# Kernel optimization log

Measured on AMD Instinct MI355X. Metric: run time of the kernel, lower is better.

## Reference

```python
import jax, jax.numpy as jnp
import numpy as np

OUT_FEATURES = 4096
IN_FEATURES = 4096
NUMEL = OUT_FEATURES * IN_FEATURES          # 16777216
NUM_SUPER = NUMEL // 256                    # 65536 superblocks of 256 weights


def setup_inputs() -> dict:
    key = jax.random.key(0)
    k_x, k_p, k_d, k_dm, k_s, k_m = jax.random.split(key, 6)
    x = jax.random.normal(k_x, (2, 2048, IN_FEATURES), dtype=jnp.float32)
    # packed bytes: two 4-bit quants per byte
    packed = jax.random.randint(k_p, (NUMEL // 2,), 0, 256, dtype=jnp.int32)
    # per-superblock fp scale/min (small positive values like real Q4_K 'd'/'dmin')
    d = jax.random.uniform(k_d, (NUM_SUPER,), dtype=jnp.float32) * 0.02
    dmin = jax.random.uniform(k_dm, (NUM_SUPER,), dtype=jnp.float32) * 0.02
    # per-subblock 6-bit scale/min quants (8 subblocks per superblock)
    scales = jax.random.randint(k_s, (NUM_SUPER * 8,), 0, 64, dtype=jnp.int32)
    mins = jax.random.randint(k_m, (NUM_SUPER * 8,), 0, 64, dtype=jnp.int32)
    return {"x": x, "packed": packed, "d": d, "dmin": dmin,
            "scales": scales, "mins": mins}


def _q4_k_dequantize(packed, d, dmin, scales, mins):
    # nibble split: low then high, interleaved per byte (stack dim=1 + flatten)
    low = packed & 15
    high = (packed >> 4) & 15
    q = jnp.stack([low, high], axis=1).reshape(-1).astype(jnp.float32)  # [NUMEL]
    blocks = q.reshape(NUM_SUPER, 8, 32)
    blk_scale = (scales.astype(jnp.float32) / 63.0).reshape(NUM_SUPER, 8, 1)
    blk_min = (mins.astype(jnp.float32) / 63.0).reshape(NUM_SUPER, 8, 1)
    normalized = blocks / 15.0 * blk_scale + blk_min
    w = normalized * d.reshape(NUM_SUPER, 1, 1) + dmin.reshape(NUM_SUPER, 1, 1)
    return w.reshape(OUT_FEATURES, IN_FEATURES)


def reference(x, packed, d, dmin, scales, mins):
    w = _q4_k_dequantize(packed, d, dmin, scales, mins).astype(x.dtype)
    # F.linear(x, w) = x @ w.T ; bias is None
    return jnp.einsum('bsk,nk->bsn', x, w)
```

## Files before the change

kernel.cpp:

```cpp
#include <hip/hip_runtime.h>
#include <stdint.h>

#define M_DIM 4096
#define K_DIM 4096
#define N_DIM 4096

typedef float f32x4 __attribute__((ext_vector_type(4)));
typedef int   i32x4 __attribute__((ext_vector_type(4)));

__global__ __launch_bounds__(256) void quant_x(const float* __restrict__ x,
                                               int8_t* __restrict__ xq,
                                               float* __restrict__ sx) {
    __shared__ float red[4];
    const int row  = blockIdx.x;
    const int base = threadIdx.x * 16;
    const float* xr = x + (size_t)row * K_DIM + base;
    float4 v[4];
#pragma unroll
    for (int c = 0; c < 4; ++c) v[c] = ((const float4*)xr)[c];
    float am = 0.f;
#pragma unroll
    for (int c = 0; c < 4; ++c) {
        am = fmaxf(am, fabsf(v[c].x)); am = fmaxf(am, fabsf(v[c].y));
        am = fmaxf(am, fabsf(v[c].z)); am = fmaxf(am, fabsf(v[c].w));
    }
#pragma unroll
    for (int off = 32; off; off >>= 1) am = fmaxf(am, __shfl_xor(am, off, 64));
    if ((threadIdx.x & 63) == 0) red[threadIdx.x >> 6] = am;
    __syncthreads();
    float amax = fmaxf(fmaxf(red[0], red[1]), fmaxf(red[2], red[3]));
    amax = fmaxf(amax, 1e-20f);
    const float inv = 127.0f / amax;
    int ow[4];
#pragma unroll
    for (int c = 0; c < 4; ++c) {
        int q0 = __float2int_rn(v[c].x * inv);
        int q1 = __float2int_rn(v[c].y * inv);
        int q2 = __float2int_rn(v[c].z * inv);
        int q3 = __float2int_rn(v[c].w * inv);
        ow[c] = (q0 & 255) | ((q1 & 255) << 8) | ((q2 & 255) << 16) | ((q3 & 255) << 24);
    }
    ((int4*)(xq + (size_t)row * K_DIM + base))[0] = make_int4(ow[0], ow[1], ow[2], ow[3]);
    if (threadIdx.x == 0) sx[row] = amax / 127.0f;
}

__global__ __launch_bounds__(256) void quant_w(const int* __restrict__ packed,
                                               const float* __restrict__ d,
                                               const float* __restrict__ dmin,
                                               const int* __restrict__ scales,
                                               const int* __restrict__ mins,
                                               int8_t* __restrict__ wq,
                                               float* __restrict__ sw) {
    __shared__ float sa[128], sb[128], red[4];
    const int n = blockIdx.x;
    const int t = threadIdx.x;
    float m = 0.f;
    if (t < 128) {
        int sub  = n * 128 + t;
        int sidx = n * 16 + (t >> 3);
        float dd = d[sidx], dm = dmin[sidx];
        float a = dd * (float)scales[sub] * (1.0f / 945.0f);
        float b = dd * (float)mins[sub] * (1.0f / 63.0f) + dm;
        sa[t] = a; sb[t] = b;
        m = 15.0f * a + b;
    }
#pragma unroll
    for (int off = 32; off; off >>= 1) m = fmaxf(m, __shfl_xor(m, off, 64));
    if ((t & 63) == 0) red[t >> 6] = m;
    __syncthreads();
    float rowmax = fmaxf(fmaxf(red[0], red[1]), fmaxf(red[2], red[3]));
    rowmax = fmaxf(rowmax, 1e-20f);
    const float inv = 127.0f / rowmax;

    const int sub = t >> 1;
    const float a = sa[sub] * inv;
    const float b = sb[sub] * inv;
    const int4* p4 = (const int4*)(packed + (size_t)n * (K_DIM / 2) + t * 8);
    int4 pv0 = p4[0], pv1 = p4[1];
    int bytes[8] = {pv0.x, pv0.y, pv0.z, pv0.w, pv1.x, pv1.y, pv1.z, pv1.w};
    int ow[4];
#pragma unroll
    for (int c = 0; c < 4; ++c) {
        int b0 = bytes[2 * c], b1 = bytes[2 * c + 1];
        int q0 = __float2int_rn((float)(b0 & 15) * a + b);
        int q1 = __float2int_rn((float)((b0 >> 4) & 15) * a + b);
        int q2 = __float2int_rn((float)(b1 & 15) * a + b);
        int q3 = __float2int_rn((float)((b1 >> 4) & 15) * a + b);
        ow[c] = (q0 & 255) | ((q1 & 255) << 8) | ((q2 & 255) << 16) | ((q3 & 255) << 24);
    }
    ((int4*)(wq + (size_t)n * K_DIM + t * 16))[0] = make_int4(ow[0], ow[1], ow[2], ow[3]);
    if (t == 0) sw[n] = rowmax / 127.0f;
}

#define BK 128

__device__ __forceinline__ void async_copy16(void* lds, const void* g) {
    __builtin_amdgcn_global_load_lds(
        (const __attribute__((address_space(1))) void*)g,
        (__attribute__((address_space(3))) void*)lds, 16, 0, 0);
}

#define BARRIER() asm volatile("s_barrier" ::: "memory")
#define LGKM0()   asm volatile("s_waitcnt lgkmcnt(0)" ::: "memory")
#define WAITV(n)  asm volatile("s_waitcnt vmcnt(" #n ")" ::: "memory")

__global__ __launch_bounds__(512, 2) void gemm_i8(const int8_t* __restrict__ A,
                                                  const int8_t* __restrict__ B,
                                                  const float* __restrict__ sx,
                                                  const float* __restrict__ sw,
                                                  float* __restrict__ C) {
    __shared__ int8_t sA[2][2][128 * 128];
    __shared__ int8_t sB[2][2][128 * 128];

    const int tid  = threadIdx.x;
    const int wave = tid >> 6;
    const int lane = tid & 63;
    const int wm = wave >> 2;
    const int wn = wave & 3;
    const int r4 = lane & 15;
    const int q  = lane >> 4;

    const int bid = blockIdx.x;
    const int lid = (bid & 7) * 32 + (bid >> 3);
    const int m0 = (lid & 15) * 256;
    const int n0 = (lid >> 4) * 256;

    i32x4 acc[2][2][4][2] = {};
    i32x4 aF[2][4], bF[2][2];

    const int rowS = tid >> 3;
    const int cS   = (tid & 7) ^ (rowS & 7);
    const size_t rs64 = (size_t)64 * K_DIM;
    const int8_t* gAh[2];
    const int8_t* gBh[2];
    gAh[0] = A + (size_t)(m0 + rowS) * K_DIM + cS * 16;
    gAh[1] = gAh[0] + (size_t)128 * K_DIM;
    gBh[0] = B + (size_t)(n0 + rowS) * K_DIM + cS * 16;
    gBh[1] = gBh[0] + (size_t)128 * K_DIM;
    const int ldsW = wave * 1024;

#define STAGE_A(buf, half, koff)                                          \
    do {                                                                  \
        async_copy16(&sA[buf][half][ldsW],        gAh[half] + (koff));    \
        async_copy16(&sA[buf][half][ldsW + 8192], gAh[half] + rs64 + (koff)); \
    } while (0)
#define STAGE_B(buf, half, koff)                                          \
    do {                                                                  \
        async_copy16(&sB[buf][half][ldsW],        gBh[half] + (koff));    \
        async_copy16(&sB[buf][half][ldsW + 8192], gBh[half] + rs64 + (koff)); \
    } while (0)

    int aOff[2][4], bOff[2][2];
#pragma unroll
    for (int ks = 0; ks < 2; ++ks) {
        const int sl = (((ks * 4 + q) ^ (r4 & 7)) * 16);
#pragma unroll
        for (int m = 0; m < 4; ++m)
            aOff[ks][m] = (wm * 64 + m * 16 + r4) * 128 + sl;
#pragma unroll
        for (int n = 0; n < 2; ++n)
            bOff[ks][n] = (wn * 32 + n * 16 + r4) * 128 + sl;
    }

#define LDA(buf, half)                                                    \
    do {                                                                  \
        _Pragma("unroll") for (int ks = 0; ks < 2; ++ks)                  \
        _Pragma("unroll") for (int m = 0; m < 4; ++m)                     \
            aF[ks][m] = *(const i32x4*)&sA[buf][half][aOff[ks][m]];       \
    } while (0)
#define LDB(buf, half)                                                    \
    do {                                                                  \
        _Pragma("unroll") for (int ks = 0; ks < 2; ++ks)                  \
        _Pragma("unroll") for (int n = 0; n < 2; ++n)                     \
            bF[ks][n] = *(const i32x4*)&sB[buf][half][bOff[ks][n]];       \
    } while (0)
#define MMA(a, b)                                                         \
    do {                                                                  \
        __builtin_amdgcn_s_setprio(1);                                    \
        _Pragma("unroll") for (int m = 0; m < 4; ++m)                     \
        _Pragma("unroll") for (int n = 0; n < 2; ++n) {                   \
            acc[a][b][m][n] = __builtin_amdgcn_mfma_i32_16x16x64_i8(      \
                aF[0][m], bF[0][n], acc[a][b][m][n], 0, 0, 0);            \
            acc[a][b][m][n] = __builtin_amdgcn_mfma_i32_16x16x64_i8(      \
                aF[1][m], bF[1][n], acc[a][b][m][n], 0, 0, 0);            \
        }                                                                 \
        __builtin_amdgcn_s_setprio(0);                                    \
    } while (0)

    STAGE_A(0, 0, 0);
    STAGE_B(0, 0, 0);
    STAGE_B(0, 1, 0);
    STAGE_A(0, 1, 0);
    STAGE_A(1, 0, BK);
    STAGE_B(1, 1, BK);
    WAITV(4);
    BARRIER();

    int ko1 = BK, ko2 = 2 * BK, ko3 = 3 * BK;
#pragma unroll 1
    for (int it = 0; it < 15; ++it) {
        LDA(0, 0); LDB(0, 0); STAGE_A(1, 1, ko1);
        BARRIER(); LGKM0(); MMA(0, 0); BARRIER();
        LDB(0, 1); STAGE_B(1, 0, ko1);
        BARRIER(); LGKM0(); MMA(0, 1); BARRIER();
        LDA(0, 1); STAGE_A(0, 0, ko2);
        BARRIER(); LGKM0(); MMA(1, 1); BARRIER();
        LDB(0, 0); STAGE_B(0, 1, ko2); WAITV(4);
        BARRIER(); LGKM0(); MMA(1, 0); BARRIER();
        LDA(1, 0); LDB(1, 0); STAGE_A(0, 1, ko2);
        BARRIER(); LGKM0(); MMA(0, 0); BARRIER();
        LDB(1, 1); STAGE_B(0, 0, ko2);
        BARRIER(); LGKM0(); MMA(0, 1); BARRIER();
        LDA(1, 1); STAGE_A(1, 0, ko3);
        BARRIER(); LGKM0(); MMA(1, 1); BARRIER();
        LDB(1, 0); STAGE_B(1, 1, ko3); WAITV(4);
        BARRIER(); LGKM0(); MMA(1, 0); BARRIER();
        ko1 += 2 * BK; ko2 += 2 * BK; ko3 += 2 * BK;
    }

    LDA(0, 0); LDB(0, 0); STAGE_A(1, 1, ko1);
    BARRIER(); LGKM0(); MMA(0, 0); BARRIER();
    LDB(0, 1); STAGE_B(1, 0, ko1);
    BARRIER(); LGKM0(); MMA(0, 1); BARRIER();
    LDA(0, 1);
    BARRIER(); LGKM0(); MMA(1, 1); BARRIER();
    LDB(0, 0); WAITV(0);
    BARRIER(); LGKM0(); MMA(1, 0); BARRIER();
    LDA(1, 0); LDB(1, 0);
    BARRIER(); LGKM0(); MMA(0, 0); BARRIER();
    LDB(1, 1);
    BARRIER(); LGKM0(); MMA(0, 1); BARRIER();
    LDA(1, 1);
    BARRIER(); LGKM0(); MMA(1, 1); BARRIER();
    LDB(1, 0);
    BARRIER(); LGKM0(); MMA(1, 0);

#pragma unroll
    for (int a = 0; a < 2; ++a)
#pragma unroll
    for (int m = 0; m < 4; ++m) {
        const int rbase = m0 + a * 128 + wm * 64 + m * 16 + q * 4;
        const float4 s4 = *(const float4*)&sx[rbase];
#pragma unroll
        for (int b = 0; b < 2; ++b)
#pragma unroll
        for (int n = 0; n < 2; ++n) {
            const int col = n0 + b * 128 + wn * 32 + n * 16 + r4;
            const float swc = sw[col];
            float* cp = C + (size_t)rbase * N_DIM + col;
            cp[0 * N_DIM] = (float)acc[a][b][m][n][0] * s4.x * swc;
            cp[1 * N_DIM] = (float)acc[a][b][m][n][1] * s4.y * swc;
            cp[2 * N_DIM] = (float)acc[a][b][m][n][2] * s4.z * swc;
            cp[3 * N_DIM] = (float)acc[a][b][m][n][3] * s4.w * swc;
        }
    }
#undef STAGE_A
#undef STAGE_B
#undef LDA
#undef LDB
#undef MMA
}

extern "C" void kernel_launch(void* const* d_in, const int* in_sizes, int n_in,
                              void* d_out, int out_size, void* d_ws, size_t ws_size,
                              hipStream_t stream) {
    const float* x      = (const float*)d_in[0];
    const int*   packed = (const int*)d_in[1];
    const float* d      = (const float*)d_in[2];
    const float* dmin   = (const float*)d_in[3];
    const int*   scales = (const int*)d_in[4];
    const int*   mins   = (const int*)d_in[5];
    float* out = (float*)d_out;

    int8_t* xq = (int8_t*)d_ws;
    int8_t* wq = xq + (size_t)M_DIM * K_DIM;
    float*  sx = (float*)(wq + (size_t)N_DIM * K_DIM);
    float*  sw = sx + M_DIM;

    quant_x<<<M_DIM, 256, 0, stream>>>(x, xq, sx);
    quant_w<<<N_DIM, 256, 0, stream>>>(packed, d, dmin, scales, mins, wq, sw);
    gemm_i8<<<256, 512, 0, stream>>>(xq, wq, sx, sw, out);
}
```

Measured before the change: 225.6 us.

## Software-pipeline LDS fragment loads into MFMA phases and halve barriers

Restructures the int8 GEMM main loop so LDS reads of the next A fragments are interleaved inside the MFMA loop, and B fragments are loaded right after each MFMA phase instead of before it. The explicit lgkmcnt(0) waits are removed and the barrier count per phase drops from two to one, with vmcnt waits loosened. This aims to hide LDS latency behind matrix instructions and cut synchronisation stalls, at the cost of more register pressure and a risk of LDS read/write hazards if the compiler-inserted waits or the single barriers do not fully order the buffer reuse.

Result: faster. 220.1 us (-2.4%).

```diff
diff --git a/kernel.cpp b/kernel.cpp
--- a/kernel.cpp
+++ b/kernel.cpp
@@ -101,7 +101,6 @@
 }
 
 #define BARRIER() asm volatile("s_barrier" ::: "memory")
-#define LGKM0()   asm volatile("s_waitcnt lgkmcnt(0)" ::: "memory")
 #define WAITV(n)  asm volatile("s_waitcnt vmcnt(" #n ")" ::: "memory")
 
 __global__ __launch_bounds__(512, 2) void gemm_i8(const int8_t* __restrict__ A,
@@ -174,7 +173,8 @@
         _Pragma("unroll") for (int n = 0; n < 2; ++n)                     \
             bF[ks][n] = *(const i32x4*)&sB[buf][half][bOff[ks][n]];       \
     } while (0)
-#define MMA(a, b)                                                         \
+
+#define MMA_Q(a, b)                                                       \
     do {                                                                  \
         __builtin_amdgcn_s_setprio(1);                                    \
         _Pragma("unroll") for (int m = 0; m < 4; ++m)                     \
@@ -187,6 +187,22 @@
         __builtin_amdgcn_s_setprio(0);                                    \
     } while (0)
 
+#define MMA_PFA(a, b, pbuf, phalf)                                        \
+    do {                                                                  \
+        __builtin_amdgcn_s_setprio(1);                                    \
+        _Pragma("unroll") for (int m = 0; m < 4; ++m) {                   \
+            _Pragma("unroll") for (int n = 0; n < 2; ++n) {               \
+                acc[a][b][m][n] = __builtin_amdgcn_mfma_i32_16x16x64_i8(  \
+                    aF[0][m], bF[0][n], acc[a][b][m][n], 0, 0, 0);        \
+                acc[a][b][m][n] = __builtin_amdgcn_mfma_i32_16x16x64_i8(  \
+                    aF[1][m], bF[1][n], acc[a][b][m][n], 0, 0, 0);        \
+            }                                                             \
+            aF[0][m] = *(const i32x4*)&sA[pbuf][phalf][aOff[0][m]];       \
+            aF[1][m] = *(const i32x4*)&sA[pbuf][phalf][aOff[1][m]];       \
+        }                                                                 \
+        __builtin_amdgcn_s_setprio(0);                                    \
+    } while (0)
+
     STAGE_A(0, 0, 0);
     STAGE_B(0, 0, 0);
     STAGE_B(0, 1, 0);
@@ -195,45 +211,70 @@
     STAGE_B(1, 1, BK);
     WAITV(4);
     BARRIER();
+    LDA(0, 0);
+    LDB(0, 0);
 
     int ko1 = BK, ko2 = 2 * BK, ko3 = 3 * BK;
 #pragma unroll 1
-    for (int it = 0; it < 15; ++it) {
-        LDA(0, 0); LDB(0, 0); STAGE_A(1, 1, ko1);
-        BARRIER(); LGKM0(); MMA(0, 0); BARRIER();
-        LDB(0, 1); STAGE_B(1, 0, ko1);
-        BARRIER(); LGKM0(); MMA(0, 1); BARRIER();
-        LDA(0, 1); STAGE_A(0, 0, ko2);
-        BARRIER(); LGKM0(); MMA(1, 1); BARRIER();
-        LDB(0, 0); STAGE_B(0, 1, ko2); WAITV(4);
-        BARRIER(); LGKM0(); MMA(1, 0); BARRIER();
-        LDA(1, 0); LDB(1, 0); STAGE_A(0, 1, ko2);
-        BARRIER(); LGKM0(); MMA(0, 0); BARRIER();
-        LDB(1, 1); STAGE_B(0, 0, ko2);
-        BARRIER(); LGKM0(); MMA(0, 1); BARRIER();
-        LDA(1, 1); STAGE_A(1, 0, ko3);
-        BARRIER(); LGKM0(); MMA(1, 1); BARRIER();
-        LDB(1, 0); STAGE_B(1, 1, ko3); WAITV(4);
-        BARRIER(); LGKM0(); MMA(1, 0); BARRIER();
+    for (int i = 0; i < 15; ++i) {
+        STAGE_A(1, 1, ko1);
+        MMA_Q(0, 0);
+        LDB(0, 1);
+        BARRIER();
+        STAGE_B(1, 0, ko1);
+        MMA_PFA(0, 1, 0, 1);
+        BARRIER();
+        STAGE_A(0, 0, ko2);
+        MMA_Q(1, 1);
+        LDB(0, 0);
+        BARRIER();
+        WAITV(2);
+        STAGE_B(0, 1, ko2);
+        MMA_PFA(1, 0, 1, 0);
+        LDB(1, 0);
+        BARRIER();
+        STAGE_A(0, 1, ko2);
+        MMA_Q(0, 0);
+        LDB(1, 1);
+        BARRIER();
+        STAGE_B(0, 0, ko2);
+        MMA_PFA(0, 1, 1, 1);
+        BARRIER();
+        STAGE_A(1, 0, ko3);
+        MMA_Q(1, 1);
+        LDB(1, 0);
+        BARRIER();
+        WAITV(2);
+        STAGE_B(1, 1, ko3);
+        MMA_PFA(1, 0, 0, 0);
+        LDB(0, 0);
+        BARRIER();
         ko1 += 2 * BK; ko2 += 2 * BK; ko3 += 2 * BK;
     }
 
-    LDA(0, 0); LDB(0, 0); STAGE_A(1, 1, ko1);
-    BARRIER(); LGKM0(); MMA(0, 0); BARRIER();
-    LDB(0, 1); STAGE_B(1, 0, ko1);
-    BARRIER(); LGKM0(); MMA(0, 1); BARRIER();
-    LDA(0, 1);
-    BARRIER(); LGKM0(); MMA(1, 1); BARRIER();
-    LDB(0, 0); WAITV(0);
-    BARRIER(); LGKM0(); MMA(1, 0); BARRIER();
-    LDA(1, 0); LDB(1, 0);
-    BARRIER(); LGKM0(); MMA(0, 0); BARRIER();
+    STAGE_A(1, 1, ko1);
+    MMA_Q(0, 0);
+    LDB(0, 1);
+    BARRIER();
+    STAGE_B(1, 0, ko1);
+    MMA_PFA(0, 1, 0, 1);
+    BARRIER();
+    MMA_Q(1, 1);
+    LDB(0, 0);
+    BARRIER();
+    WAITV(0);
+    MMA_PFA(1, 0, 1, 0);
+    LDB(1, 0);
+    BARRIER();
+    MMA_Q(0, 0);
     LDB(1, 1);
-    BARRIER(); LGKM0(); MMA(0, 1); BARRIER();
-    LDA(1, 1);
-    BARRIER(); LGKM0(); MMA(1, 1); BARRIER();
+    BARRIER();
+    MMA_PFA(0, 1, 1, 1);
+    BARRIER();
+    MMA_Q(1, 1);
     LDB(1, 0);
-    BARRIER(); LGKM0(); MMA(1, 0);
+    BARRIER();
+    MMA_Q(1, 0);
 
 #pragma unroll
     for (int a = 0; a < 2; ++a)
@@ -258,7 +299,8 @@
 #undef STAGE_B
 #undef LDA
 #undef LDB
-#undef MMA
+#undef MMA_Q
+#undef MMA_PFA
 }
 
 extern "C" void kernel_launch(void* const* d_in, const int* in_sizes, int n_in,
```

## Switch GEMM to 32x32x32 MFMA with interleaved LDS reads and merge quant kernels

Applied to the files above, without the earlier changes.

The int8 GEMM moves from 16x16x64 to 32x32x32 MFMA tiles, which raises arithmetic per fragment load. It is restructured so that LDS fragment reads for the next sub-tile are interleaved with the MFMAs, replacing the earlier barrier/lgkmcnt(0) load-then-compute phases. The x and weight quantization kernels are merged into one launch to save a kernel launch gap. The tighter software pipeline removes the explicit lgkmcnt waits and depends on the compiler inserting correct waits, and it raises register pressure.

New measurement: 356.6 us. 1.58x slower.

```diff
diff --git a/kernel.cpp b/kernel.cpp
--- a/kernel.cpp
+++ b/kernel.cpp
@@ -5,91 +5,92 @@
 #define K_DIM 4096
 #define N_DIM 4096
 
-typedef float f32x4 __attribute__((ext_vector_type(4)));
-typedef int   i32x4 __attribute__((ext_vector_type(4)));
-
-__global__ __launch_bounds__(256) void quant_x(const float* __restrict__ x,
-                                               int8_t* __restrict__ xq,
-                                               float* __restrict__ sx) {
-    __shared__ float red[4];
-    const int row  = blockIdx.x;
-    const int base = threadIdx.x * 16;
-    const float* xr = x + (size_t)row * K_DIM + base;
-    float4 v[4];
-#pragma unroll
-    for (int c = 0; c < 4; ++c) v[c] = ((const float4*)xr)[c];
-    float am = 0.f;
-#pragma unroll
-    for (int c = 0; c < 4; ++c) {
-        am = fmaxf(am, fabsf(v[c].x)); am = fmaxf(am, fabsf(v[c].y));
-        am = fmaxf(am, fabsf(v[c].z)); am = fmaxf(am, fabsf(v[c].w));
-    }
-#pragma unroll
-    for (int off = 32; off; off >>= 1) am = fmaxf(am, __shfl_xor(am, off, 64));
-    if ((threadIdx.x & 63) == 0) red[threadIdx.x >> 6] = am;
-    __syncthreads();
-    float amax = fmaxf(fmaxf(red[0], red[1]), fmaxf(red[2], red[3]));
-    amax = fmaxf(amax, 1e-20f);
-    const float inv = 127.0f / amax;
-    int ow[4];
-#pragma unroll
-    for (int c = 0; c < 4; ++c) {
-        int q0 = __float2int_rn(v[c].x * inv);
-        int q1 = __float2int_rn(v[c].y * inv);
-        int q2 = __float2int_rn(v[c].z * inv);
-        int q3 = __float2int_rn(v[c].w * inv);
-        ow[c] = (q0 & 255) | ((q1 & 255) << 8) | ((q2 & 255) << 16) | ((q3 & 255) << 24);
-    }
-    ((int4*)(xq + (size_t)row * K_DIM + base))[0] = make_int4(ow[0], ow[1], ow[2], ow[3]);
-    if (threadIdx.x == 0) sx[row] = amax / 127.0f;
-}
-
-__global__ __launch_bounds__(256) void quant_w(const int* __restrict__ packed,
-                                               const float* __restrict__ d,
-                                               const float* __restrict__ dmin,
-                                               const int* __restrict__ scales,
-                                               const int* __restrict__ mins,
-                                               int8_t* __restrict__ wq,
-                                               float* __restrict__ sw) {
+typedef float f32x4  __attribute__((ext_vector_type(4)));
+typedef int   i32x4  __attribute__((ext_vector_type(4)));
+typedef int   i32x16 __attribute__((ext_vector_type(16)));
+
+__global__ __launch_bounds__(256) void quant_xw(const float* __restrict__ x,
+                                                const int* __restrict__ packed,
+                                                const float* __restrict__ d,
+                                                const float* __restrict__ dmin,
+                                                const int* __restrict__ scales,
+                                                const int* __restrict__ mins,
+                                                int8_t* __restrict__ xq,
+                                                float* __restrict__ sx,
+                                                int8_t* __restrict__ wq,
+                                                float* __restrict__ sw) {
     __shared__ float sa[128], sb[128], red[4];
-    const int n = blockIdx.x;
-    const int t = threadIdx.x;
-    float m = 0.f;
-    if (t < 128) {
-        int sub  = n * 128 + t;
-        int sidx = n * 16 + (t >> 3);
-        float dd = d[sidx], dm = dmin[sidx];
-        float a = dd * (float)scales[sub] * (1.0f / 945.0f);
-        float b = dd * (float)mins[sub] * (1.0f / 63.0f) + dm;
-        sa[t] = a; sb[t] = b;
-        m = 15.0f * a + b;
-    }
-#pragma unroll
-    for (int off = 32; off; off >>= 1) m = fmaxf(m, __shfl_xor(m, off, 64));
-    if ((t & 63) == 0) red[t >> 6] = m;
-    __syncthreads();
-    float rowmax = fmaxf(fmaxf(red[0], red[1]), fmaxf(red[2], red[3]));
-    rowmax = fmaxf(rowmax, 1e-20f);
-    const float inv = 127.0f / rowmax;
-
-    const int sub = t >> 1;
-    const float a = sa[sub] * inv;
-    const float b = sb[sub] * inv;
-    const int4* p4 = (const int4*)(packed + (size_t)n * (K_DIM / 2) + t * 8);
-    int4 pv0 = p4[0], pv1 = p4[1];
-    int bytes[8] = {pv0.x, pv0.y, pv0.z, pv0.w, pv1.x, pv1.y, pv1.z, pv1.w};
-    int ow[4];
-#pragma unroll
-    for (int c = 0; c < 4; ++c) {
-        int b0 = bytes[2 * c], b1 = bytes[2 * c + 1];
-        int q0 = __float2int_rn((float)(b0 & 15) * a + b);
-        int q1 = __float2int_rn((float)((b0 >> 4) & 15) * a + b);
-        int q2 = __float2int_rn((float)(b1 & 15) * a + b);
-        int q3 = __float2int_rn((float)((b1 >> 4) & 15) * a + b);
-        ow[c] = (q0 & 255) | ((q1 & 255) << 8) | ((q2 & 255) << 16) | ((q3 & 255) << 24);
-    }
-    ((int4*)(wq + (size_t)n * K_DIM + t * 16))[0] = make_int4(ow[0], ow[1], ow[2], ow[3]);
-    if (t == 0) sw[n] = rowmax / 127.0f;
+    if (blockIdx.x < 4096) {
+        const int row  = blockIdx.x;
+        const int base = threadIdx.x * 16;
+        const float* xr = x + (size_t)row * K_DIM + base;
+        float4 v[4];
+#pragma unroll
+        for (int c = 0; c < 4; ++c) v[c] = ((const float4*)xr)[c];
+        float am = 0.f;
+#pragma unroll
+        for (int c = 0; c < 4; ++c) {
+            am = fmaxf(am, fabsf(v[c].x)); am = fmaxf(am, fabsf(v[c].y));
+            am = fmaxf(am, fabsf(v[c].z)); am = fmaxf(am, fabsf(v[c].w));
+        }
+#pragma unroll
+        for (int off = 32; off; off >>= 1) am = fmaxf(am, __shfl_xor(am, off, 64));
+        if ((threadIdx.x & 63) == 0) red[threadIdx.x >> 6] = am;
+        __syncthreads();
+        float amax = fmaxf(fmaxf(red[0], red[1]), fmaxf(red[2], red[3]));
+        amax = fmaxf(amax, 1e-20f);
+        const float inv = 127.0f / amax;
+        int ow[4];
+#pragma unroll
+        for (int c = 0; c < 4; ++c) {
+            int q0 = __float2int_rn(v[c].x * inv);
+            int q1 = __float2int_rn(v[c].y * inv);
+            int q2 = __float2int_rn(v[c].z * inv);
+            int q3 = __float2int_rn(v[c].w * inv);
+            ow[c] = (q0 & 255) | ((q1 & 255) << 8) | ((q2 & 255) << 16) | ((q3 & 255) << 24);
+        }
+        ((int4*)(xq + (size_t)row * K_DIM + base))[0] = make_int4(ow[0], ow[1], ow[2], ow[3]);
+        if (threadIdx.x == 0) sx[row] = amax / 127.0f;
+    } else {
+        const int n = blockIdx.x - 4096;
+        const int t = threadIdx.x;
+        float m = 0.f;
+        if (t < 128) {
+            int sub  = n * 128 + t;
+            int sidx = n * 16 + (t >> 3);
+            float dd = d[sidx], dm = dmin[sidx];
+            float a = dd * (float)scales[sub] * (1.0f / 945.0f);
+            float b = dd * (float)mins[sub] * (1.0f / 63.0f) + dm;
+            sa[t] = a; sb[t] = b;
+            m = 15.0f * a + b;
+        }
+#pragma unroll
+        for (int off = 32; off; off >>= 1) m = fmaxf(m, __shfl_xor(m, off, 64));
+        if ((t & 63) == 0) red[t >> 6] = m;
+        __syncthreads();
+        float rowmax = fmaxf(fmaxf(red[0], red[1]), fmaxf(red[2], red[3]));
+        rowmax = fmaxf(rowmax, 1e-20f);
+        const float inv = 127.0f / rowmax;
+
+        const int sub = t >> 1;
+        const float a = sa[sub] * inv;
+        const float b = sb[sub] * inv;
+        const int4* p4 = (const int4*)(packed + (size_t)n * (K_DIM / 2) + t * 8);
+        int4 pv0 = p4[0], pv1 = p4[1];
+        int bytes[8] = {pv0.x, pv0.y, pv0.z, pv0.w, pv1.x, pv1.y, pv1.z, pv1.w};
+        int ow[4];
+#pragma unroll
+        for (int c = 0; c < 4; ++c) {
+            int b0 = bytes[2 * c], b1 = bytes[2 * c + 1];
+            int q0 = __float2int_rn((float)(b0 & 15) * a + b);
+            int q1 = __float2int_rn((float)((b0 >> 4) & 15) * a + b);
+            int q2 = __float2int_rn((float)(b1 & 15) * a + b);
+            int q3 = __float2int_rn((float)((b1 >> 4) & 15) * a + b);
+            ow[c] = (q0 & 255) | ((q1 & 255) << 8) | ((q2 & 255) << 16) | ((q3 & 255) << 24);
+        }
+        ((int4*)(wq + (size_t)n * K_DIM + t * 16))[0] = make_int4(ow[0], ow[1], ow[2], ow[3]);
+        if (t == 0) sw[n] = rowmax / 127.0f;
+    }
 }
 
 #define BK 128
@@ -101,8 +102,8 @@
 }
 
 #define BARRIER() asm volatile("s_barrier" ::: "memory")
-#define LGKM0()   asm volatile("s_waitcnt lgkmcnt(0)" ::: "memory")
 #define WAITV(n)  asm volatile("s_waitcnt vmcnt(" #n ")" ::: "memory")
+#define mfma32(a, b, c) __builtin_amdgcn_mfma_i32_32x32x32_i8(a, b, c, 0, 0, 0)
 
 __global__ __launch_bounds__(512, 2) void gemm_i8(const int8_t* __restrict__ A,
                                                   const int8_t* __restrict__ B,
@@ -115,18 +116,19 @@
     const int tid  = threadIdx.x;
     const int wave = tid >> 6;
     const int lane = tid & 63;
-    const int wm = wave >> 2;
-    const int wn = wave & 3;
-    const int r4 = lane & 15;
-    const int q  = lane >> 4;
+    const int wm  = wave >> 2;
+    const int wn  = wave & 3;
+    const int l31 = lane & 31;
+    const int hi  = lane >> 5;
 
     const int bid = blockIdx.x;
     const int lid = (bid & 7) * 32 + (bid >> 3);
     const int m0 = (lid & 15) * 256;
     const int n0 = (lid >> 4) * 256;
 
-    i32x4 acc[2][2][4][2] = {};
-    i32x4 aF[2][4], bF[2][2];
+    i32x16 acc[2][2][2] = {};
+    i32x4  aF[2][4];
+    i32x4  bF0[4], bF1[4];
 
     const int rowS = tid >> 3;
     const int cS   = (tid & 7) ^ (rowS & 7);
@@ -150,39 +152,68 @@
         async_copy16(&sB[buf][half][ldsW + 8192], gBh[half] + rs64 + (koff)); \
     } while (0)
 
-    int aOff[2][4], bOff[2][2];
-#pragma unroll
-    for (int ks = 0; ks < 2; ++ks) {
-        const int sl = (((ks * 4 + q) ^ (r4 & 7)) * 16);
-#pragma unroll
-        for (int m = 0; m < 4; ++m)
-            aOff[ks][m] = (wm * 64 + m * 16 + r4) * 128 + sl;
-#pragma unroll
-        for (int n = 0; n < 2; ++n)
-            bOff[ks][n] = (wn * 32 + n * 16 + r4) * 128 + sl;
-    }
-
-#define LDA(buf, half)                                                    \
-    do {                                                                  \
-        _Pragma("unroll") for (int ks = 0; ks < 2; ++ks)                  \
-        _Pragma("unroll") for (int m = 0; m < 4; ++m)                     \
-            aF[ks][m] = *(const i32x4*)&sA[buf][half][aOff[ks][m]];       \
-    } while (0)
-#define LDB(buf, half)                                                    \
-    do {                                                                  \
-        _Pragma("unroll") for (int ks = 0; ks < 2; ++ks)                  \
-        _Pragma("unroll") for (int n = 0; n < 2; ++n)                     \
-            bF[ks][n] = *(const i32x4*)&sB[buf][half][bOff[ks][n]];       \
-    } while (0)
-#define MMA(a, b)                                                         \
+    int aOff[2][4], bOff[4];
+#pragma unroll
+    for (int mb = 0; mb < 2; ++mb) {
+        const int r = wm * 64 + mb * 32 + l31;
+#pragma unroll
+        for (int ks = 0; ks < 4; ++ks)
+            aOff[mb][ks] = r * 128 + (((ks * 2 + hi) ^ (r & 7)) * 16);
+    }
+    {
+        const int r = wn * 32 + l31;
+#pragma unroll
+        for (int ks = 0; ks < 4; ++ks)
+            bOff[ks] = r * 128 + (((ks * 2 + hi) ^ (r & 7)) * 16);
+    }
+
+#define RD_A(buf, half, mb, ks) (*(const i32x4*)&sA[buf][half][aOff[mb][ks]])
+#define RD_B(buf, half, ks)     (*(const i32x4*)&sB[buf][half][bOff[ks]])
+
+#define PH_A(tb)                                                          \
     do {                                                                  \
         __builtin_amdgcn_s_setprio(1);                                    \
-        _Pragma("unroll") for (int m = 0; m < 4; ++m)                     \
-        _Pragma("unroll") for (int n = 0; n < 2; ++n) {                   \
-            acc[a][b][m][n] = __builtin_amdgcn_mfma_i32_16x16x64_i8(      \
-                aF[0][m], bF[0][n], acc[a][b][m][n], 0, 0, 0);            \
-            acc[a][b][m][n] = __builtin_amdgcn_mfma_i32_16x16x64_i8(      \
-                aF[1][m], bF[1][n], acc[a][b][m][n], 0, 0, 0);            \
+        _Pragma("unroll") for (int ks = 0; ks < 4; ++ks) {                \
+            acc[0][0][0] = mfma32(aF[0][ks], bF0[ks], acc[0][0][0]);      \
+            acc[0][0][1] = mfma32(aF[1][ks], bF0[ks], acc[0][0][1]);      \
+        }                                                                 \
+        _Pragma("unroll") for (int ks = 0; ks < 4; ++ks) {                \
+            acc[0][1][0] = mfma32(aF[0][ks], bF1[ks], acc[0][1][0]);      \
+            aF[0][ks] = RD_A(tb, 1, 0, ks);                               \
+            acc[0][1][1] = mfma32(aF[1][ks], bF1[ks], acc[0][1][1]);      \
+            aF[1][ks] = RD_A(tb, 1, 1, ks);                               \
+        }                                                                 \
+        __builtin_amdgcn_s_setprio(0);                                    \
+    } while (0)
+
+#define PH_B(nbuf)                                                        \
+    do {                                                                  \
+        __builtin_amdgcn_s_setprio(1);                                    \
+        _Pragma("unroll") for (int ks = 0; ks < 4; ++ks) {                \
+            acc[1][1][0] = mfma32(aF[0][ks], bF1[ks], acc[1][1][0]);      \
+            acc[1][1][1] = mfma32(aF[1][ks], bF1[ks], acc[1][1][1]);      \
+            bF1[ks] = RD_B(nbuf, 1, ks);                                  \
+        }                                                                 \
+        _Pragma("unroll") for (int ks = 0; ks < 4; ++ks) {                \
+            acc[1][0][0] = mfma32(aF[0][ks], bF0[ks], acc[1][0][0]);      \
+            aF[0][ks] = RD_A(nbuf, 0, 0, ks);                             \
+            acc[1][0][1] = mfma32(aF[1][ks], bF0[ks], acc[1][0][1]);      \
+            aF[1][ks] = RD_A(nbuf, 0, 1, ks);                             \
+            bF0[ks] = RD_B(nbuf, 0, ks);                                  \
+        }                                                                 \
+        __builtin_amdgcn_s_setprio(0);                                    \
+    } while (0)
+
+#define PH_B_END()                                                        \
+    do {                                                                  \
+        __builtin_amdgcn_s_setprio(1);                                    \
+        _Pragma("unroll") for (int ks = 0; ks < 4; ++ks) {                \
+            acc[1][1][0] = mfma32(aF[0][ks], bF1[ks], acc[1][1][0]);      \
+            acc[1][1][1] = mfma32(aF[1][ks], bF1[ks], acc[1][1][1]);      \
+        }                                                                 \
+        _Pragma("unroll") for (int ks = 0; ks < 4; ++ks) {                \
+            acc[1][0][0] = mfma32(aF[0][ks], bF0[ks], acc[1][0][0]);      \
+            acc[1][0][1] = mfma32(aF[1][ks], bF0[ks], acc[1][0][1]);      \
         }                                                                 \
         __builtin_amdgcn_s_setprio(0);                                    \
     } while (0)
@@ -192,73 +223,78 @@
     STAGE_B(0, 1, 0);
     STAGE_A(0, 1, 0);
     STAGE_A(1, 0, BK);
-    STAGE_B(1, 1, BK);
+    STAGE_B(1, 0, BK);
     WAITV(4);
     BARRIER();
-
-    int ko1 = BK, ko2 = 2 * BK, ko3 = 3 * BK;
+#pragma unroll
+    for (int mb = 0; mb < 2; ++mb)
+#pragma unroll
+        for (int ks = 0; ks < 4; ++ks) aF[mb][ks] = RD_A(0, 0, mb, ks);
+#pragma unroll
+    for (int ks = 0; ks < 4; ++ks) { bF0[ks] = RD_B(0, 0, ks); bF1[ks] = RD_B(0, 1, ks); }
+
+    int koB1 = BK, koU2 = 2 * BK, koV2 = 3 * BK;
 #pragma unroll 1
-    for (int it = 0; it < 15; ++it) {
-        LDA(0, 0); LDB(0, 0); STAGE_A(1, 1, ko1);
-        BARRIER(); LGKM0(); MMA(0, 0); BARRIER();
-        LDB(0, 1); STAGE_B(1, 0, ko1);
-        BARRIER(); LGKM0(); MMA(0, 1); BARRIER();
-        LDA(0, 1); STAGE_A(0, 0, ko2);
-        BARRIER(); LGKM0(); MMA(1, 1); BARRIER();
-        LDB(0, 0); STAGE_B(0, 1, ko2); WAITV(4);
-        BARRIER(); LGKM0(); MMA(1, 0); BARRIER();
-        LDA(1, 0); LDB(1, 0); STAGE_A(0, 1, ko2);
-        BARRIER(); LGKM0(); MMA(0, 0); BARRIER();
-        LDB(1, 1); STAGE_B(0, 0, ko2);
-        BARRIER(); LGKM0(); MMA(0, 1); BARRIER();
-        LDA(1, 1); STAGE_A(1, 0, ko3);
-        BARRIER(); LGKM0(); MMA(1, 1); BARRIER();
-        LDB(1, 0); STAGE_B(1, 1, ko3); WAITV(4);
-        BARRIER(); LGKM0(); MMA(1, 0); BARRIER();
-        ko1 += 2 * BK; ko2 += 2 * BK; ko3 += 2 * BK;
-    }
-
-    LDA(0, 0); LDB(0, 0); STAGE_A(1, 1, ko1);
-    BARRIER(); LGKM0(); MMA(0, 0); BARRIER();
-    LDB(0, 1); STAGE_B(1, 0, ko1);
-    BARRIER(); LGKM0(); MMA(0, 1); BARRIER();
-    LDA(0, 1);
-    BARRIER(); LGKM0(); MMA(1, 1); BARRIER();
-    LDB(0, 0); WAITV(0);
-    BARRIER(); LGKM0(); MMA(1, 0); BARRIER();
-    LDA(1, 0); LDB(1, 0);
-    BARRIER(); LGKM0(); MMA(0, 0); BARRIER();
-    LDB(1, 1);
-    BARRIER(); LGKM0(); MMA(0, 1); BARRIER();
-    LDA(1, 1);
-    BARRIER(); LGKM0(); MMA(1, 1); BARRIER();
-    LDB(1, 0);
-    BARRIER(); LGKM0(); MMA(1, 0);
+    for (int j = 0; j < 15; ++j) {
+        WAITV(4);
+        STAGE_B(1, 1, koB1); STAGE_A(1, 1, koB1);
+        PH_A(0);
+        BARRIER();
+        WAITV(2);
+        STAGE_A(0, 0, koU2); STAGE_B(0, 0, koU2);
+        PH_B(1);
+        BARRIER();
+        WAITV(4);
+        STAGE_B(0, 1, koU2); STAGE_A(0, 1, koU2);
+        PH_A(1);
+        BARRIER();
+        WAITV(2);
+        STAGE_A(1, 0, koV2); STAGE_B(1, 0, koV2);
+        PH_B(0);
+        BARRIER();
+        koB1 += 2 * BK; koU2 += 2 * BK; koV2 += 2 * BK;
+    }
+
+    WAITV(4);
+    STAGE_B(1, 1, koB1); STAGE_A(1, 1, koB1);
+    PH_A(0);
+    BARRIER();
+    WAITV(2);
+    PH_B(1);
+    BARRIER();
+    WAITV(0);
+    PH_A(1);
+    BARRIER();
+    PH_B_END();
 
 #pragma unroll
     for (int a = 0; a < 2; ++a)
 #pragma unroll
-    for (int m = 0; m < 4; ++m) {
-        const int rbase = m0 + a * 128 + wm * 64 + m * 16 + q * 4;
-        const float4 s4 = *(const float4*)&sx[rbase];
-#pragma unroll
-        for (int b = 0; b < 2; ++b)
-#pragma unroll
-        for (int n = 0; n < 2; ++n) {
-            const int col = n0 + b * 128 + wn * 32 + n * 16 + r4;
+    for (int mb = 0; mb < 2; ++mb) {
+        const int row0 = m0 + a * 128 + wm * 64 + mb * 32 + hi * 4;
+#pragma unroll
+        for (int b = 0; b < 2; ++b) {
+            const int col = n0 + b * 128 + wn * 32 + l31;
             const float swc = sw[col];
-            float* cp = C + (size_t)rbase * N_DIM + col;
-            cp[0 * N_DIM] = (float)acc[a][b][m][n][0] * s4.x * swc;
-            cp[1 * N_DIM] = (float)acc[a][b][m][n][1] * s4.y * swc;
-            cp[2 * N_DIM] = (float)acc[a][b][m][n][2] * s4.z * swc;
-            cp[3 * N_DIM] = (float)acc[a][b][m][n][3] * s4.w * swc;
+#pragma unroll
+            for (int g = 0; g < 4; ++g) {
+                const int rbase = row0 + 8 * g;
+                const float4 s4 = *(const float4*)&sx[rbase];
+                float* cp = C + (size_t)rbase * N_DIM + col;
+                cp[0 * N_DIM] = (float)acc[a][b][mb][4 * g + 0] * s4.x * swc;
+                cp[1 * N_DIM] = (float)acc[a][b][mb][4 * g + 1] * s4.y * swc;
+                cp[2 * N_DIM] = (float)acc[a][b][mb][4 * g + 2] * s4.z * swc;
+                cp[3 * N_DIM] = (float)acc[a][b][mb][4 * g + 3] * s4.w * swc;
+            }
         }
     }
 #undef STAGE_A
 #undef STAGE_B
-#undef LDA
-#undef LDB
-#undef MMA
+#undef RD_A
+#undef RD_B
+#undef PH_A
+#undef PH_B
+#undef PH_B_END
 }
 
 extern "C" void kernel_launch(void* const* d_in, const int* in_sizes, int n_in,
@@ -277,7 +313,7 @@
     float*  sx = (float*)(wq + (size_t)N_DIM * K_DIM);
     float*  sw = sx + M_DIM;
 
-    quant_x<<<M_DIM, 256, 0, stream>>>(x, xq, sx);
-    quant_w<<<N_DIM, 256, 0, stream>>>(packed, d, dmin, scales, mins, wq, sw);
+    quant_xw<<<8192, 256, 0, stream>>>(x, packed, d, dmin, scales, mins,
+                                       xq, sx, wq, sw);
     gemm_i8<<<256, 512, 0, stream>>>(xq, wq, sx, sw, out);
 }
```

## Restructure int8 GEMM warp tiling with interleaved LDS reads and merge quant kernels

Applied to the files above, without the earlier changes.

The GEMM changes its wave layout from 2x4 to 4x2 waves, so each wave now owns a 64x128 output tile. LDS fragment reads for the next B/A group are interleaved with the MFMA calls, and the schedule drops from eight barrier pairs per two K-steps to two barriers per tile. The two quantization kernels are merged into one launch of 8192 blocks, which removes one kernel launch. The costs are higher register pressure from 32 accumulators per wave and a more intricate double-buffer hazard ordering.

After: 215.4 us. 1.05x faster.

```diff
diff --git a/kernel.cpp b/kernel.cpp
--- a/kernel.cpp
+++ b/kernel.cpp
@@ -8,88 +8,88 @@
 typedef float f32x4 __attribute__((ext_vector_type(4)));
 typedef int   i32x4 __attribute__((ext_vector_type(4)));
 
-__global__ __launch_bounds__(256) void quant_x(const float* __restrict__ x,
-                                               int8_t* __restrict__ xq,
-                                               float* __restrict__ sx) {
-    __shared__ float red[4];
-    const int row  = blockIdx.x;
-    const int base = threadIdx.x * 16;
-    const float* xr = x + (size_t)row * K_DIM + base;
-    float4 v[4];
-#pragma unroll
-    for (int c = 0; c < 4; ++c) v[c] = ((const float4*)xr)[c];
-    float am = 0.f;
-#pragma unroll
-    for (int c = 0; c < 4; ++c) {
-        am = fmaxf(am, fabsf(v[c].x)); am = fmaxf(am, fabsf(v[c].y));
-        am = fmaxf(am, fabsf(v[c].z)); am = fmaxf(am, fabsf(v[c].w));
-    }
-#pragma unroll
-    for (int off = 32; off; off >>= 1) am = fmaxf(am, __shfl_xor(am, off, 64));
-    if ((threadIdx.x & 63) == 0) red[threadIdx.x >> 6] = am;
-    __syncthreads();
-    float amax = fmaxf(fmaxf(red[0], red[1]), fmaxf(red[2], red[3]));
-    amax = fmaxf(amax, 1e-20f);
-    const float inv = 127.0f / amax;
-    int ow[4];
-#pragma unroll
-    for (int c = 0; c < 4; ++c) {
-        int q0 = __float2int_rn(v[c].x * inv);
-        int q1 = __float2int_rn(v[c].y * inv);
-        int q2 = __float2int_rn(v[c].z * inv);
-        int q3 = __float2int_rn(v[c].w * inv);
-        ow[c] = (q0 & 255) | ((q1 & 255) << 8) | ((q2 & 255) << 16) | ((q3 & 255) << 24);
-    }
-    ((int4*)(xq + (size_t)row * K_DIM + base))[0] = make_int4(ow[0], ow[1], ow[2], ow[3]);
-    if (threadIdx.x == 0) sx[row] = amax / 127.0f;
-}
-
-__global__ __launch_bounds__(256) void quant_w(const int* __restrict__ packed,
-                                               const float* __restrict__ d,
-                                               const float* __restrict__ dmin,
-                                               const int* __restrict__ scales,
-                                               const int* __restrict__ mins,
-                                               int8_t* __restrict__ wq,
-                                               float* __restrict__ sw) {
+__global__ __launch_bounds__(256) void quant_xw(const float* __restrict__ x,
+                                                const int* __restrict__ packed,
+                                                const float* __restrict__ d,
+                                                const float* __restrict__ dmin,
+                                                const int* __restrict__ scales,
+                                                const int* __restrict__ mins,
+                                                int8_t* __restrict__ xq,
+                                                float* __restrict__ sx,
+                                                int8_t* __restrict__ wq,
+                                                float* __restrict__ sw) {
     __shared__ float sa[128], sb[128], red[4];
-    const int n = blockIdx.x;
-    const int t = threadIdx.x;
-    float m = 0.f;
-    if (t < 128) {
-        int sub  = n * 128 + t;
-        int sidx = n * 16 + (t >> 3);
-        float dd = d[sidx], dm = dmin[sidx];
-        float a = dd * (float)scales[sub] * (1.0f / 945.0f);
-        float b = dd * (float)mins[sub] * (1.0f / 63.0f) + dm;
-        sa[t] = a; sb[t] = b;
-        m = 15.0f * a + b;
-    }
-#pragma unroll
-    for (int off = 32; off; off >>= 1) m = fmaxf(m, __shfl_xor(m, off, 64));
-    if ((t & 63) == 0) red[t >> 6] = m;
-    __syncthreads();
-    float rowmax = fmaxf(fmaxf(red[0], red[1]), fmaxf(red[2], red[3]));
-    rowmax = fmaxf(rowmax, 1e-20f);
-    const float inv = 127.0f / rowmax;
-
-    const int sub = t >> 1;
-    const float a = sa[sub] * inv;
-    const float b = sb[sub] * inv;
-    const int4* p4 = (const int4*)(packed + (size_t)n * (K_DIM / 2) + t * 8);
-    int4 pv0 = p4[0], pv1 = p4[1];
-    int bytes[8] = {pv0.x, pv0.y, pv0.z, pv0.w, pv1.x, pv1.y, pv1.z, pv1.w};
-    int ow[4];
-#pragma unroll
-    for (int c = 0; c < 4; ++c) {
-        int b0 = bytes[2 * c], b1 = bytes[2 * c + 1];
-        int q0 = __float2int_rn((float)(b0 & 15) * a + b);
-        int q1 = __float2int_rn((float)((b0 >> 4) & 15) * a + b);
-        int q2 = __float2int_rn((float)(b1 & 15) * a + b);
-        int q3 = __float2int_rn((float)((b1 >> 4) & 15) * a + b);
-        ow[c] = (q0 & 255) | ((q1 & 255) << 8) | ((q2 & 255) << 16) | ((q3 & 255) << 24);
-    }
-    ((int4*)(wq + (size_t)n * K_DIM + t * 16))[0] = make_int4(ow[0], ow[1], ow[2], ow[3]);
-    if (t == 0) sw[n] = rowmax / 127.0f;
+    if (blockIdx.x < 4096) {
+        const int row  = blockIdx.x;
+        const int base = threadIdx.x * 16;
+        const float* xr = x + (size_t)row * K_DIM + base;
+        float4 v[4];
+#pragma unroll
+        for (int c = 0; c < 4; ++c) v[c] = ((const float4*)xr)[c];
+        float am = 0.f;
+#pragma unroll
+        for (int c = 0; c < 4; ++c) {
+            am = fmaxf(am, fabsf(v[c].x)); am = fmaxf(am, fabsf(v[c].y));
+            am = fmaxf(am, fabsf(v[c].z)); am = fmaxf(am, fabsf(v[c].w));
+        }
+#pragma unroll
+        for (int off = 32; off; off >>= 1) am = fmaxf(am, __shfl_xor(am, off, 64));
+        if ((threadIdx.x & 63) == 0) red[threadIdx.x >> 6] = am;
+        __syncthreads();
+        float amax = fmaxf(fmaxf(red[0], red[1]), fmaxf(red[2], red[3]));
+        amax = fmaxf(amax, 1e-20f);
+        const float inv = 127.0f / amax;
+        int ow[4];
+#pragma unroll
+        for (int c = 0; c < 4; ++c) {
+            int q0 = __float2int_rn(v[c].x * inv);
+            int q1 = __float2int_rn(v[c].y * inv);
+            int q2 = __float2int_rn(v[c].z * inv);
+            int q3 = __float2int_rn(v[c].w * inv);
+            ow[c] = (q0 & 255) | ((q1 & 255) << 8) | ((q2 & 255) << 16) | ((q3 & 255) << 24);
+        }
+        ((int4*)(xq + (size_t)row * K_DIM + base))[0] = make_int4(ow[0], ow[1], ow[2], ow[3]);
+        if (threadIdx.x == 0) sx[row] = amax / 127.0f;
+    } else {
+        const int n = blockIdx.x - 4096;
+        const int t = threadIdx.x;
+        float m = 0.f;
+        if (t < 128) {
+            int sub  = n * 128 + t;
+            int sidx = n * 16 + (t >> 3);
+            float dd = d[sidx], dm = dmin[sidx];
+            float a = dd * (float)scales[sub] * (1.0f / 945.0f);
+            float b = dd * (float)mins[sub] * (1.0f / 63.0f) + dm;
+            sa[t] = a; sb[t] = b;
+            m = 15.0f * a + b;
+        }
+#pragma unroll
+        for (int off = 32; off; off >>= 1) m = fmaxf(m, __shfl_xor(m, off, 64));
+        if ((t & 63) == 0) red[t >> 6] = m;
+        __syncthreads();
+        float rowmax = fmaxf(fmaxf(red[0], red[1]), fmaxf(red[2], red[3]));
+        rowmax = fmaxf(rowmax, 1e-20f);
+        const float inv = 127.0f / rowmax;
+
+        const int sub = t >> 1;
+        const float a = sa[sub] * inv;
+        const float b = sb[sub] * inv;
+        const int4* p4 = (const int4*)(packed + (size_t)n * (K_DIM / 2) + t * 8);
+        int4 pv0 = p4[0], pv1 = p4[1];
+        int bytes[8] = {pv0.x, pv0.y, pv0.z, pv0.w, pv1.x, pv1.y, pv1.z, pv1.w};
+        int ow[4];
+#pragma unroll
+        for (int c = 0; c < 4; ++c) {
+            int b0 = bytes[2 * c], b1 = bytes[2 * c + 1];
+            int q0 = __float2int_rn((float)(b0 & 15) * a + b);
+            int q1 = __float2int_rn((float)((b0 >> 4) & 15) * a + b);
+            int q2 = __float2int_rn((float)(b1 & 15) * a + b);
+            int q3 = __float2int_rn((float)((b1 >> 4) & 15) * a + b);
+            ow[c] = (q0 & 255) | ((q1 & 255) << 8) | ((q2 & 255) << 16) | ((q3 & 255) << 24);
+        }
+        ((int4*)(wq + (size_t)n * K_DIM + t * 16))[0] = make_int4(ow[0], ow[1], ow[2], ow[3]);
+        if (t == 0) sw[n] = rowmax / 127.0f;
+    }
 }
 
 #define BK 128
@@ -101,8 +101,9 @@
 }
 
 #define BARRIER() asm volatile("s_barrier" ::: "memory")
+#define WAITV(n)  asm volatile("s_waitcnt vmcnt(" #n ")" ::: "memory")
 #define LGKM0()   asm volatile("s_waitcnt lgkmcnt(0)" ::: "memory")
-#define WAITV(n)  asm volatile("s_waitcnt vmcnt(" #n ")" ::: "memory")
+#define mfma64(a, b, c) __builtin_amdgcn_mfma_i32_16x16x64_i8(a, b, c, 0, 0, 0)
 
 __global__ __launch_bounds__(512, 2) void gemm_i8(const int8_t* __restrict__ A,
                                                   const int8_t* __restrict__ B,
@@ -115,18 +116,20 @@
     const int tid  = threadIdx.x;
     const int wave = tid >> 6;
     const int lane = tid & 63;
-    const int wm = wave >> 2;
-    const int wn = wave & 3;
+    const int wm = wave >> 1;
+    const int wn = wave & 1;
     const int r4 = lane & 15;
     const int q  = lane >> 4;
+    const int ah = wm >> 1;
 
     const int bid = blockIdx.x;
     const int lid = (bid & 7) * 32 + (bid >> 3);
     const int m0 = (lid & 15) * 256;
     const int n0 = (lid >> 4) * 256;
 
-    i32x4 acc[2][2][4][2] = {};
-    i32x4 aF[2][4], bF[2][2];
+    i32x4 acc[4][8] = {};
+    i32x4 aF[2][4];
+    i32x4 bFa[2][2], bFb[2][2];
 
     const int rowS = tid >> 3;
     const int cS   = (tid & 7) ^ (rowS & 7);
@@ -150,115 +153,121 @@
         async_copy16(&sB[buf][half][ldsW + 8192], gBh[half] + rs64 + (koff)); \
     } while (0)
 
-    int aOff[2][4], bOff[2][2];
+    int aOffB[2], bOffB[2];
 #pragma unroll
     for (int ks = 0; ks < 2; ++ks) {
         const int sl = (((ks * 4 + q) ^ (r4 & 7)) * 16);
-#pragma unroll
-        for (int m = 0; m < 4; ++m)
-            aOff[ks][m] = (wm * 64 + m * 16 + r4) * 128 + sl;
-#pragma unroll
-        for (int n = 0; n < 2; ++n)
-            bOff[ks][n] = (wn * 32 + n * 16 + r4) * 128 + sl;
-    }
-
-#define LDA(buf, half)                                                    \
-    do {                                                                  \
-        _Pragma("unroll") for (int ks = 0; ks < 2; ++ks)                  \
-        _Pragma("unroll") for (int m = 0; m < 4; ++m)                     \
-            aF[ks][m] = *(const i32x4*)&sA[buf][half][aOff[ks][m]];       \
-    } while (0)
-#define LDB(buf, half)                                                    \
-    do {                                                                  \
-        _Pragma("unroll") for (int ks = 0; ks < 2; ++ks)                  \
-        _Pragma("unroll") for (int n = 0; n < 2; ++n)                     \
-            bF[ks][n] = *(const i32x4*)&sB[buf][half][bOff[ks][n]];       \
-    } while (0)
-#define MMA(a, b)                                                         \
+        aOffB[ks] = ((wm & 1) * 64 + r4) * 128 + sl;
+        bOffB[ks] = r4 * 128 + sl;
+    }
+
+#define RD_A(buf, ks, m) (*(const i32x4*)&sA[buf][ah][aOffB[ks] + (m) * 2048])
+#define RD_B(buf, ks, n) (*(const i32x4*)&sB[buf][wn][bOffB[ks] + (n) * 2048])
+
+#define MMA_BW(g, BC, BN, rb, ng)                                         \
+    do {                                                                  \
+        __builtin_amdgcn_s_setprio(1);                                    \
+        _Pragma("unroll") for (int m = 0; m < 4; ++m) {                   \
+            _Pragma("unroll") for (int nn = 0; nn < 2; ++nn) {            \
+                acc[m][2*(g)+nn] = mfma64(aF[0][m], BC[0][nn], acc[m][2*(g)+nn]); \
+                acc[m][2*(g)+nn] = mfma64(aF[1][m], BC[1][nn], acc[m][2*(g)+nn]); \
+            }                                                             \
+            BN[m & 1][m >> 1] = RD_B(rb, m & 1, 2*(ng) + (m >> 1));       \
+        }                                                                 \
+        __builtin_amdgcn_s_setprio(0);                                    \
+    } while (0)
+
+#define MMA_P4(BC, BN, nb)                                                \
+    do {                                                                  \
+        __builtin_amdgcn_s_setprio(1);                                    \
+        _Pragma("unroll") for (int m = 0; m < 4; ++m) {                   \
+            _Pragma("unroll") for (int nn = 0; nn < 2; ++nn) {            \
+                acc[m][6+nn] = mfma64(aF[0][m], BC[0][nn], acc[m][6+nn]); \
+                acc[m][6+nn] = mfma64(aF[1][m], BC[1][nn], acc[m][6+nn]); \
+            }                                                             \
+            aF[0][m] = RD_A(nb, 0, m);                                    \
+            aF[1][m] = RD_A(nb, 1, m);                                    \
+            BN[m & 1][m >> 1] = RD_B(nb, m & 1, (m >> 1));                \
+        }                                                                 \
+        __builtin_amdgcn_s_setprio(0);                                    \
+    } while (0)
+
+#define MMA_END(BC)                                                       \
     do {                                                                  \
         __builtin_amdgcn_s_setprio(1);                                    \
         _Pragma("unroll") for (int m = 0; m < 4; ++m)                     \
-        _Pragma("unroll") for (int n = 0; n < 2; ++n) {                   \
-            acc[a][b][m][n] = __builtin_amdgcn_mfma_i32_16x16x64_i8(      \
-                aF[0][m], bF[0][n], acc[a][b][m][n], 0, 0, 0);            \
-            acc[a][b][m][n] = __builtin_amdgcn_mfma_i32_16x16x64_i8(      \
-                aF[1][m], bF[1][n], acc[a][b][m][n], 0, 0, 0);            \
+        _Pragma("unroll") for (int nn = 0; nn < 2; ++nn) {                \
+            acc[m][6+nn] = mfma64(aF[0][m], BC[0][nn], acc[m][6+nn]);     \
+            acc[m][6+nn] = mfma64(aF[1][m], BC[1][nn], acc[m][6+nn]);     \
         }                                                                 \
         __builtin_amdgcn_s_setprio(0);                                    \
     } while (0)
 
-    STAGE_A(0, 0, 0);
-    STAGE_B(0, 0, 0);
-    STAGE_B(0, 1, 0);
-    STAGE_A(0, 1, 0);
-    STAGE_A(1, 0, BK);
-    STAGE_B(1, 1, BK);
-    WAITV(4);
+#define TILE(p, koA, koB)                                                 \
+    do {                                                                  \
+        STAGE_B((p)^1, 0, koB); STAGE_B((p)^1, 1, koB); STAGE_A(p, 0, koA); \
+        MMA_BW(0, bFa, bFb, p, 1);                                        \
+        STAGE_A(p, 1, koA);                                               \
+        MMA_BW(1, bFb, bFa, p, 2);                                        \
+        WAITV(2); BARRIER();                                              \
+        MMA_BW(2, bFa, bFb, p, 3);                                        \
+        MMA_P4(bFb, bFa, (p)^1);                                          \
+        WAITV(2); BARRIER();                                              \
+    } while (0)
+
+    STAGE_A(0, 0, 0); STAGE_A(0, 1, 0); STAGE_B(0, 0, 0); STAGE_B(0, 1, 0);
+    WAITV(0);
     BARRIER();
-
-    int ko1 = BK, ko2 = 2 * BK, ko3 = 3 * BK;
+#pragma unroll
+    for (int m = 0; m < 4; ++m) { aF[0][m] = RD_A(0, 0, m); aF[1][m] = RD_A(0, 1, m); }
+#pragma unroll
+    for (int nn = 0; nn < 2; ++nn) { bFa[0][nn] = RD_B(0, 0, nn); bFa[1][nn] = RD_B(0, 1, nn); }
+    LGKM0();
+    BARRIER();
+    STAGE_A(1, 0, BK); STAGE_A(1, 1, BK);
+
 #pragma unroll 1
-    for (int it = 0; it < 15; ++it) {
-        LDA(0, 0); LDB(0, 0); STAGE_A(1, 1, ko1);
-        BARRIER(); LGKM0(); MMA(0, 0); BARRIER();
-        LDB(0, 1); STAGE_B(1, 0, ko1);
-        BARRIER(); LGKM0(); MMA(0, 1); BARRIER();
-        LDA(0, 1); STAGE_A(0, 0, ko2);
-        BARRIER(); LGKM0(); MMA(1, 1); BARRIER();
-        LDB(0, 0); STAGE_B(0, 1, ko2); WAITV(4);
-        BARRIER(); LGKM0(); MMA(1, 0); BARRIER();
-        LDA(1, 0); LDB(1, 0); STAGE_A(0, 1, ko2);
-        BARRIER(); LGKM0(); MMA(0, 0); BARRIER();
-        LDB(1, 1); STAGE_B(0, 0, ko2);
-        BARRIER(); LGKM0(); MMA(0, 1); BARRIER();
-        LDA(1, 1); STAGE_A(1, 0, ko3);
-        BARRIER(); LGKM0(); MMA(1, 1); BARRIER();
-        LDB(1, 0); STAGE_B(1, 1, ko3); WAITV(4);
-        BARRIER(); LGKM0(); MMA(1, 0); BARRIER();
-        ko1 += 2 * BK; ko2 += 2 * BK; ko3 += 2 * BK;
-    }
-
-    LDA(0, 0); LDB(0, 0); STAGE_A(1, 1, ko1);
-    BARRIER(); LGKM0(); MMA(0, 0); BARRIER();
-    LDB(0, 1); STAGE_B(1, 0, ko1);
-    BARRIER(); LGKM0(); MMA(0, 1); BARRIER();
-    LDA(0, 1);
-    BARRIER(); LGKM0(); MMA(1, 1); BARRIER();
-    LDB(0, 0); WAITV(0);
-    BARRIER(); LGKM0(); MMA(1, 0); BARRIER();
-    LDA(1, 0); LDB(1, 0);
-    BARRIER(); LGKM0(); MMA(0, 0); BARRIER();
-    LDB(1, 1);
-    BARRIER(); LGKM0(); MMA(0, 1); BARRIER();
-    LDA(1, 1);
-    BARRIER(); LGKM0(); MMA(1, 1); BARRIER();
-    LDB(1, 0);
-    BARRIER(); LGKM0(); MMA(1, 0);
-
-#pragma unroll
-    for (int a = 0; a < 2; ++a)
+    for (int i = 0; i < 15; ++i) {
+        const int t2 = 2 * i;
+        TILE(0, (t2 + 2) * BK, (t2 + 1) * BK);
+        TILE(1, (t2 + 3) * BK, (t2 + 2) * BK);
+    }
+
+    STAGE_B(1, 0, 31 * BK); STAGE_B(1, 1, 31 * BK);
+    MMA_BW(0, bFa, bFb, 0, 1);
+    MMA_BW(1, bFb, bFa, 0, 2);
+    WAITV(2); BARRIER();
+    MMA_BW(2, bFa, bFb, 0, 3);
+    MMA_P4(bFb, bFa, 1);
+    WAITV(0); BARRIER();
+    MMA_BW(0, bFa, bFb, 1, 1);
+    MMA_BW(1, bFb, bFa, 1, 2);
+    MMA_BW(2, bFa, bFb, 1, 3);
+    MMA_END(bFb);
+
 #pragma unroll
     for (int m = 0; m < 4; ++m) {
-        const int rbase = m0 + a * 128 + wm * 64 + m * 16 + q * 4;
+        const int rbase = m0 + wm * 64 + m * 16 + q * 4;
         const float4 s4 = *(const float4*)&sx[rbase];
 #pragma unroll
-        for (int b = 0; b < 2; ++b)
-#pragma unroll
-        for (int n = 0; n < 2; ++n) {
-            const int col = n0 + b * 128 + wn * 32 + n * 16 + r4;
+        for (int n = 0; n < 8; ++n) {
+            const int col = n0 + wn * 128 + n * 16 + r4;
             const float swc = sw[col];
             float* cp = C + (size_t)rbase * N_DIM + col;
-            cp[0 * N_DIM] = (float)acc[a][b][m][n][0] * s4.x * swc;
-            cp[1 * N_DIM] = (float)acc[a][b][m][n][1] * s4.y * swc;
-            cp[2 * N_DIM] = (float)acc[a][b][m][n][2] * s4.z * swc;
-            cp[3 * N_DIM] = (float)acc[a][b][m][n][3] * s4.w * swc;
+            cp[0 * N_DIM] = (float)acc[m][n][0] * s4.x * swc;
+            cp[1 * N_DIM] = (float)acc[m][n][1] * s4.y * swc;
+            cp[2 * N_DIM] = (float)acc[m][n][2] * s4.z * swc;
+            cp[3 * N_DIM] = (float)acc[m][n][3] * s4.w * swc;
         }
     }
 #undef STAGE_A
 #undef STAGE_B
-#undef LDA
-#undef LDB
-#undef MMA
+#undef RD_A
+#undef RD_B
+#undef MMA_BW
+#undef MMA_P4
+#undef MMA_END
+#undef TILE
 }
 
 extern "C" void kernel_launch(void* const* d_in, const int* in_sizes, int n_in,
@@ -277,7 +286,7 @@
     float*  sx = (float*)(wq + (size_t)N_DIM * K_DIM);
     float*  sw = sx + M_DIM;
 
-    quant_x<<<M_DIM, 256, 0, stream>>>(x, xq, sx);
-    quant_w<<<N_DIM, 256, 0, stream>>>(packed, d, dmin, scales, mins, wq, sw);
+    quant_xw<<<8192, 256, 0, stream>>>(x, packed, d, dmin, scales, mins,
+                                       xq, sx, wq, sw);
     gemm_i8<<<256, 512, 0, stream>>>(xq, wq, sx, sw, out);
 }
```
